# Optimization experiments

Measured on AMD Instinct MI355X. Metric: run time of the kernel, lower is better.

## Reference

```python
import jax, jax.numpy as jnp
import numpy as np

N_GRAPHS = 256
NEG_SLOPE = 0.2


def _add_self_loops(src, dst, edge_attr, n):
    # PyG fill_value='mean': self-loop edge_attr = per-node mean of incoming edge_attr
    sums = jax.ops.segment_sum(edge_attr, dst, num_segments=n)
    cnt = jax.ops.segment_sum(jnp.ones((dst.shape[0],), edge_attr.dtype), dst, num_segments=n)
    loop_attr = sums / jnp.maximum(cnt, 1.0)[:, None]
    loop = jnp.arange(n)
    src = jnp.concatenate([src, loop])
    dst = jnp.concatenate([dst, loop])
    ea = jnp.concatenate([edge_attr, loop_attr], axis=0)
    return src, dst, ea


def _segment_softmax(scores, seg, n):
    # scores: [E, H]; softmax over edges sharing the same target node
    m = jax.ops.segment_max(scores, seg, num_segments=n)
    ex = jnp.exp(scores - m[seg])
    s = jax.ops.segment_sum(ex, seg, num_segments=n)
    return ex / jnp.maximum(s[seg], 1e-16)


def gatv2_layer(x, src, dst, ea, w_l, w_r, w_e, att, b, heads, out_ch, concat):
    n = x.shape[0]
    x_l = (x @ w_l).reshape(n, heads, out_ch)  # source transform
    x_r = (x @ w_r).reshape(n, heads, out_ch)  # target transform
    e_f = (ea @ w_e).reshape(-1, heads, out_ch)
    m = x_l[src] + x_r[dst] + e_f                               # [E, H, C]
    score = jnp.einsum('ehc,hc->eh', jax.nn.leaky_relu(m, NEG_SLOPE), att)
    alpha = _segment_softmax(score, dst, n)                      # [E, H]
    out = jax.ops.segment_sum(alpha[:, :, None] * x_l[src], dst, num_segments=n)
    if concat:
        return out.reshape(n, heads * out_ch) + b
    return out.mean(axis=1) + b


def reference(x, edge_index, edge_attr, batch,
              w_l1, w_r1, w_e1, att1, b1,
              w_l2, w_r2, w_e2, att2, b2,
              w_fc, b_fc):
    n = x.shape[0]
    src, dst, ea = _add_self_loops(edge_index[0], edge_index[1], edge_attr, n)
    h = gatv2_layer(x, src, dst, ea, w_l1, w_r1, w_e1, att1, b1, heads=2, out_ch=32, concat=True)
    h = jax.nn.relu(h)
    h = gatv2_layer(h, src, dst, ea, w_l2, w_r2, w_e2, att2, b2, heads=1, out_ch=32, concat=False)
    h = jax.nn.relu(h)
    # global mean pool over graphs
    sums = jax.ops.segment_sum(h, batch, num_segments=N_GRAPHS)
    cnt = jax.ops.segment_sum(jnp.ones((n,), h.dtype), batch, num_segments=N_GRAPHS)
    pooled = sums / jnp.maximum(cnt, 1.0)[:, None]
    return pooled @ w_fc + b_fc


def setup_inputs() -> dict:
    key = jax.random.key(0)
    ks = jax.random.split(key, 20)
    N, E, IN, H, C, ED, OUT = 100000, 1600000, 128, 2, 32, 16, 32
    s = 0.05
    return {
        'x': jax.random.normal(ks[0], (N, IN), jnp.float32),
        'edge_index': jax.random.randint(ks[1], (2, E), 0, N, jnp.int32),
        'edge_attr': jax.random.normal(ks[2], (E, ED), jnp.float32),
        'batch': jnp.sort(jax.random.randint(ks[3], (N,), 0, 256, jnp.int32)),
        'w_l1': jax.random.normal(ks[4], (IN, H * C), jnp.float32) * s,
        'w_r1': jax.random.normal(ks[5], (IN, H * C), jnp.float32) * s,
        'w_e1': jax.random.normal(ks[6], (ED, H * C), jnp.float32) * s,
        'att1': jax.random.normal(ks[7], (H, C), jnp.float32) * s,
        'b1': jnp.zeros((H * C,), jnp.float32),
        'w_l2': jax.random.normal(ks[8], (H * C, C), jnp.float32) * s,
        'w_r2': jax.random.normal(ks[9], (H * C, C), jnp.float32) * s,
        'w_e2': jax.random.normal(ks[10], (ED, C), jnp.float32) * s,
        'att2': jax.random.normal(ks[11], (1, C), jnp.float32) * s,
        'b2': jnp.zeros((C,), jnp.float32),
        'w_fc': jax.random.normal(ks[12], (C, OUT), jnp.float32) * s,
        'b_fc': jnp.zeros((OUT,), jnp.float32),
    }
```

## Files before the change

### kernel.cpp

```cpp
#include <hip/hip_runtime.h>
#include <hip/hip_bf16.h>
#include <hip/hip_fp16.h>

#define NEG_SLOPE 0.2f
#define LOG2E 1.4426950408889634f

typedef _Float16 h2v __attribute__((ext_vector_type(2)));
typedef __fp16 f16x2 __attribute__((ext_vector_type(2)));
union hu { h2v h; f16x2 f; unsigned int u; };

__global__ void scan1_k(const int* __restrict__ deg, int* __restrict__ rowptr,
                        int* __restrict__ aux, int N) {
  __shared__ int sh[256];
  int t = threadIdx.x, i = blockIdx.x * 256 + t;
  int v = (i < N) ? deg[i] : 0;
  sh[t] = v; __syncthreads();
  for (int off = 1; off < 256; off <<= 1) {
    int x = (t >= off) ? sh[t - off] : 0;
    __syncthreads();
    sh[t] += x;
    __syncthreads();
  }
  if (i < N) rowptr[i] = sh[t] - v;
  if (t == 255) aux[blockIdx.x] = sh[255];
}

__global__ void scan2_k(int* __restrict__ aux, int naux) {
  __shared__ int sh[512];
  int t = threadIdx.x;
  int v = (t < naux) ? aux[t] : 0;
  sh[t] = v; __syncthreads();
  for (int off = 1; off < 512; off <<= 1) {
    int x = (t >= off) ? sh[t - off] : 0;
    __syncthreads();
    sh[t] += x;
    __syncthreads();
  }
  if (t < naux) aux[t] = sh[t] - v;
}

__global__ void scan3_k(int* __restrict__ rowptr, int* __restrict__ cursor,
                        const int* __restrict__ aux, int N, int E) {
  int i = blockIdx.x * blockDim.x + threadIdx.x;
  if (i < N) {
    int r = rowptr[i] + aux[i >> 8];
    rowptr[i] = r;
    cursor[i] = r;
  } else if (i == N) {
    rowptr[N] = E;
  }
}

__global__ void scatter_k(const int* __restrict__ srcA, const int* __restrict__ dstA,
                          const float* __restrict__ ea, int* __restrict__ cursor,
                          int* __restrict__ csr_src, uint4* __restrict__ ea_h, int E) {
  int e = blockIdx.x * blockDim.x + threadIdx.x;
  if (e >= E) return;
  int pos = atomicAdd(&cursor[dstA[e]], 1);
  csr_src[pos] = srcA[e];
  const float* p = ea + (size_t)e * 16;
  union { __half2 h2[8]; uint4 u[2]; } cv;
#pragma unroll
  for (int k = 0; k < 8; ++k) cv.h2[k] = __floats2half2_rn(p[2 * k], p[2 * k + 1]);
  uint4* d = ea_h + (size_t)pos * 2;
  d[0] = cv.u[0];
  d[1] = cv.u[1];
}

__global__ __launch_bounds__(256) void t1deg_k(
    const float* __restrict__ x, const float* __restrict__ wl, const float* __restrict__ wr,
    float* __restrict__ xl, float* __restrict__ xr, int N,
    const int* __restrict__ dstA, int* __restrict__ deg, int E, int degBlocks) {
  __shared__ unsigned int wS[64 * 128];
  __shared__ unsigned int xs[32 * 64];
  int t = threadIdx.x;
  if ((int)blockIdx.x < degBlocks) {
    int base = blockIdx.x * 1024 + t;
#pragma unroll
    for (int k = 0; k < 4; ++k) {
      int e = base + k * 256;
      if (e < E) atomicAdd(&deg[dstA[e]], 1);
    }
    return;
  }
  int tile = blockIdx.x - degBlocks;
  for (int i = t; i < 64 * 64; i += 256) {
    int kp = i >> 6, j = i & 63;
    hu pl, pr;
    pl.f = __builtin_amdgcn_cvt_pkrtz(wl[(2 * kp) * 64 + j], wl[(2 * kp + 1) * 64 + j]);
    pr.f = __builtin_amdgcn_cvt_pkrtz(wr[(2 * kp) * 64 + j], wr[(2 * kp + 1) * 64 + j]);
    wS[kp * 128 + j]      = pl.u;
    wS[kp * 128 + 64 + j] = pr.u;
  }
  {
    int base = tile << 5;
    const float4* x4 = (const float4*)x;
    for (int i = t; i < 1024; i += 256) {
      int node = base + (i >> 5);
      float4 v = {0.f, 0.f, 0.f, 0.f};
      if (node < N) v = x4[(size_t)node * 32 + (i & 31)];
      hu p0, p1;
      p0.f = __builtin_amdgcn_cvt_pkrtz(v.x, v.y);
      p1.f = __builtin_amdgcn_cvt_pkrtz(v.z, v.w);
      uint2* d = (uint2*)&xs[(i >> 5) * 64 + (i & 31) * 2];
      *d = make_uint2(p0.u, p1.u);
    }
    __syncthreads();
    int tc = t & 31;
    int tr = t >> 5;
    float4 acc0 = {0,0,0,0}, acc1 = {0,0,0,0}, acc2 = {0,0,0,0}, acc3 = {0,0,0,0};
    const unsigned int* xrow = &xs[tr * 4 * 64];
#pragma unroll 4
    for (int kp = 0; kp < 64; ++kp) {
      uint4 wu = *(const uint4*)&wS[kp * 128 + tc * 4];
      hu w0, w1, w2, w3, q0, q1, q2, q3;
      w0.u = wu.x; w1.u = wu.y; w2.u = wu.z; w3.u = wu.w;
      q0.u = xrow[kp]; q1.u = xrow[64 + kp]; q2.u = xrow[128 + kp]; q3.u = xrow[192 + kp];
      acc0.x = __builtin_amdgcn_fdot2(q0.h, w0.h, acc0.x, false);
      acc0.y = __builtin_amdgcn_fdot2(q0.h, w1.h, acc0.y, false);
      acc0.z = __builtin_amdgcn_fdot2(q0.h, w2.h, acc0.z, false);
      acc0.w = __builtin_amdgcn_fdot2(q0.h, w3.h, acc0.w, false);
      acc1.x = __builtin_amdgcn_fdot2(q1.h, w0.h, acc1.x, false);
      acc1.y = __builtin_amdgcn_fdot2(q1.h, w1.h, acc1.y, false);
      acc1.z = __builtin_amdgcn_fdot2(q1.h, w2.h, acc1.z, false);
      acc1.w = __builtin_amdgcn_fdot2(q1.h, w3.h, acc1.w, false);
      acc2.x = __builtin_amdgcn_fdot2(q2.h, w0.h, acc2.x, false);
      acc2.y = __builtin_amdgcn_fdot2(q2.h, w1.h, acc2.y, false);
      acc2.z = __builtin_amdgcn_fdot2(q2.h, w2.h, acc2.z, false);
      acc2.w = __builtin_amdgcn_fdot2(q2.h, w3.h, acc2.w, false);
      acc3.x = __builtin_amdgcn_fdot2(q3.h, w0.h, acc3.x, false);
      acc3.y = __builtin_amdgcn_fdot2(q3.h, w1.h, acc3.y, false);
      acc3.z = __builtin_amdgcn_fdot2(q3.h, w2.h, acc3.z, false);
      acc3.w = __builtin_amdgcn_fdot2(q3.h, w3.h, acc3.w, false);
    }
    float* dp = (tc < 16) ? xl : xr;
    int j4 = (tc & 15) * 4;
    int nb = base + tr * 4;
    if (nb + 0 < N) *(float4*)&dp[(size_t)(nb + 0) * 64 + j4] = acc0;
    if (nb + 1 < N) *(float4*)&dp[(size_t)(nb + 1) * 64 + j4] = acc1;
    if (nb + 2 < N) *(float4*)&dp[(size_t)(nb + 2) * 64 + j4] = acc2;
    if (nb + 3 < N) *(float4*)&dp[(size_t)(nb + 3) * 64 + j4] = acc3;
  }
}

__global__ __launch_bounds__(256) void transform2_k(
    const float* __restrict__ h, const float* __restrict__ wl, const float* __restrict__ wr,
    float* __restrict__ xl, float* __restrict__ xr, int N) {
  __shared__ unsigned int wS[32 * 64];
  __shared__ unsigned int xs[64 * 32];
  int t = threadIdx.x;
  for (int i = t; i < 32 * 32; i += 256) {
    int kp = i >> 5, j = i & 31;
    hu pl, pr;
    pl.f = __builtin_amdgcn_cvt_pkrtz(wl[(2 * kp) * 32 + j], wl[(2 * kp + 1) * 32 + j]);
    pr.f = __builtin_amdgcn_cvt_pkrtz(wr[(2 * kp) * 32 + j], wr[(2 * kp + 1) * 32 + j]);
    wS[kp * 64 + j]      = pl.u;
    wS[kp * 64 + 32 + j] = pr.u;
  }
  {
    int tile = blockIdx.x;
    int base = tile << 6;
    const float4* h4 = (const float4*)h;
    for (int i = t; i < 1024; i += 256) {
      int node = base + (i >> 4);
      float4 v = {0.f, 0.f, 0.f, 0.f};
      if (node < N) v = h4[(size_t)node * 16 + (i & 15)];
      hu p0, p1;
      p0.f = __builtin_amdgcn_cvt_pkrtz(v.x, v.y);
      p1.f = __builtin_amdgcn_cvt_pkrtz(v.z, v.w);
      uint2* d = (uint2*)&xs[(i >> 4) * 32 + (i & 15) * 2];
      *d = make_uint2(p0.u, p1.u);
    }
    __syncthreads();
    int tc = t & 15;
    int tr = t >> 4;
    float4 acc0 = {0,0,0,0}, acc1 = {0,0,0,0}, acc2 = {0,0,0,0}, acc3 = {0,0,0,0};
    const unsigned int* xrow = &xs[tr * 4 * 32];
#pragma unroll 4
    for (int kp = 0; kp < 32; ++kp) {
      uint4 wu = *(const uint4*)&wS[kp * 64 + tc * 4];
      hu w0, w1, w2, w3, q0, q1, q2, q3;
      w0.u = wu.x; w1.u = wu.y; w2.u = wu.z; w3.u = wu.w;
      q0.u = xrow[kp]; q1.u = xrow[32 + kp]; q2.u = xrow[64 + kp]; q3.u = xrow[96 + kp];
      acc0.x = __builtin_amdgcn_fdot2(q0.h, w0.h, acc0.x, false);
      acc0.y = __builtin_amdgcn_fdot2(q0.h, w1.h, acc0.y, false);
      acc0.z = __builtin_amdgcn_fdot2(q0.h, w2.h, acc0.z, false);
      acc0.w = __builtin_amdgcn_fdot2(q0.h, w3.h, acc0.w, false);
      acc1.x = __builtin_amdgcn_fdot2(q1.h, w0.h, acc1.x, false);
      acc1.y = __builtin_amdgcn_fdot2(q1.h, w1.h, acc1.y, false);
      acc1.z = __builtin_amdgcn_fdot2(q1.h, w2.h, acc1.z, false);
      acc1.w = __builtin_amdgcn_fdot2(q1.h, w3.h, acc1.w, false);
      acc2.x = __builtin_amdgcn_fdot2(q2.h, w0.h, acc2.x, false);
      acc2.y = __builtin_amdgcn_fdot2(q2.h, w1.h, acc2.y, false);
      acc2.z = __builtin_amdgcn_fdot2(q2.h, w2.h, acc2.z, false);
      acc2.w = __builtin_amdgcn_fdot2(q2.h, w3.h, acc2.w, false);
      acc3.x = __builtin_amdgcn_fdot2(q3.h, w0.h, acc3.x, false);
      acc3.y = __builtin_amdgcn_fdot2(q3.h, w1.h, acc3.y, false);
      acc3.z = __builtin_amdgcn_fdot2(q3.h, w2.h, acc3.z, false);
      acc3.w = __builtin_amdgcn_fdot2(q3.h, w3.h, acc3.w, false);
    }
    float* dp = (tc < 8) ? xl : xr;
    int j4 = (tc & 7) * 4;
    int nb = base + tr * 4;
    if (nb + 0 < N) *(float4*)&dp[(size_t)(nb + 0) * 32 + j4] = acc0;
    if (nb + 1 < N) *(float4*)&dp[(size_t)(nb + 1) * 32 + j4] = acc1;
    if (nb + 2 < N) *(float4*)&dp[(size_t)(nb + 2) * 32 + j4] = acc2;
    if (nb + 3 < N) *(float4*)&dp[(size_t)(nb + 3) * 32 + j4] = acc3;
  }
}

__global__ __launch_bounds__(256) void gat1_k(
    const int* __restrict__ rowptr, const int* __restrict__ csr_src,
    const uint4* __restrict__ ea_h, const float* __restrict__ we,
    const float* __restrict__ att, const float* __restrict__ b,
    const float* __restrict__ xl, const float* __restrict__ xr,
    float* __restrict__ h, int N) {
  int t = threadIdx.x;
  int lane = t & 63;
  h2v wh[8];
#pragma unroll
  for (int k = 0; k < 8; ++k) {
    wh[k].x = (_Float16)we[(2 * k) * 64 + lane];
    wh[k].y = (_Float16)we[(2 * k + 1) * 64 + lane];
  }
  float att_r = att[lane] * LOG2E;
  float b_r = b[lane];
  int wid = (blockIdx.x * blockDim.x + t) >> 6;
  int n0 = wid * 4;
  for (int jj = 0; jj < 4; ++jj) {
    int n = n0 + jj;
    if (n >= N) break;
    float xr_v = xr[(size_t)n * 64 + lane];
    float xl_s = xl[(size_t)n * 64 + lane];
    float num = 0.f, den = 0.f, efsum = 0.f;
    int rs = __builtin_amdgcn_readfirstlane(rowptr[n]);
    int re = __builtin_amdgcn_readfirstlane(rowptr[n + 1]);
    for (int base = rs; base < re; base += 64) {
      int cnt = min(64, re - base);
      int s_l = 0;
      if (lane < cnt) s_l = csr_src[base + lane];
      int i = 0;
      for (; i + 1 < cnt; i += 2) {
        int sa = __builtin_amdgcn_readlane(s_l, i);
        int sb = __builtin_amdgcn_readlane(s_l, i + 1);
        const float* pa = xl + (size_t)sa * 64;
        const float* pb = xl + (size_t)sb * 64;
        float xa = pa[lane];
        float xb = pb[lane];
        const uint4* epa = ea_h + (size_t)(base + i) * 2;
        union { uint4 u; h2v h[4]; } a0, a1, c0, c1;
        a0.u = epa[0]; a1.u = epa[1];
        c0.u = epa[2]; c1.u = epa[3];
        float fa0 = 0.f, fa1 = 0.f, fb0 = 0.f, fb1 = 0.f;
        fa0 = __builtin_amdgcn_fdot2(a0.h[0], wh[0], fa0, false);
        fb0 = __builtin_amdgcn_fdot2(c0.h[0], wh[0], fb0, false);
        fa1 = __builtin_amdgcn_fdot2(a0.h[1], wh[1], fa1, false);
        fb1 = __builtin_amdgcn_fdot2(c0.h[1], wh[1], fb1, false);
        fa0 = __builtin_amdgcn_fdot2(a0.h[2], wh[2], fa0, false);
        fb0 = __builtin_amdgcn_fdot2(c0.h[2], wh[2], fb0, false);
        fa1 = __builtin_amdgcn_fdot2(a0.h[3], wh[3], fa1, false);
        fb1 = __builtin_amdgcn_fdot2(c0.h[3], wh[3], fb1, false);
        fa0 = __builtin_amdgcn_fdot2(a1.h[0], wh[4], fa0, false);
        fb0 = __builtin_amdgcn_fdot2(c1.h[0], wh[4], fb0, false);
        fa1 = __builtin_amdgcn_fdot2(a1.h[1], wh[5], fa1, false);
        fb1 = __builtin_amdgcn_fdot2(c1.h[1], wh[5], fb1, false);
        fa0 = __builtin_amdgcn_fdot2(a1.h[2], wh[6], fa0, false);
        fb0 = __builtin_amdgcn_fdot2(c1.h[2], wh[6], fb0, false);
        fa1 = __builtin_amdgcn_fdot2(a1.h[3], wh[7], fa1, false);
        fb1 = __builtin_amdgcn_fdot2(c1.h[3], wh[7], fb1, false);
        float fa = fa0 + fa1, fb = fb0 + fb1;
        float ma = xa + xr_v + fa; ma = fmaxf(ma, NEG_SLOPE * ma);
        float mb = xb + xr_v + fb; mb = fmaxf(mb, NEG_SLOPE * mb);
        float ta = ma * att_r, tb = mb * att_r;
#pragma unroll
        for (int off = 1; off < 32; off <<= 1) {
          ta += __shfl_xor(ta, off);
          tb += __shfl_xor(tb, off);
        }
        float ga = __builtin_amdgcn_exp2f(ta), gb = __builtin_amdgcn_exp2f(tb);
        num += ga * xa + gb * xb;
        den += ga + gb;
        efsum += fa + fb;
      }
      if (i < cnt) {
        int sa = __builtin_amdgcn_readlane(s_l, i);
        const float* pa = xl + (size_t)sa * 64;
        float xa = pa[lane];
        const uint4* epa = ea_h + (size_t)(base + i) * 2;
        union { uint4 u; h2v h[4]; } a0, a1;
        a0.u = epa[0]; a1.u = epa[1];
        float fa0 = 0.f, fa1 = 0.f;
        fa0 = __builtin_amdgcn_fdot2(a0.h[0], wh[0], fa0, false);
        fa1 = __builtin_amdgcn_fdot2(a0.h[1], wh[1], fa1, false);
        fa0 = __builtin_amdgcn_fdot2(a0.h[2], wh[2], fa0, false);
        fa1 = __builtin_amdgcn_fdot2(a0.h[3], wh[3], fa1, false);
        fa0 = __builtin_amdgcn_fdot2(a1.h[0], wh[4], fa0, false);
        fa1 = __builtin_amdgcn_fdot2(a1.h[1], wh[5], fa1, false);
        fa0 = __builtin_amdgcn_fdot2(a1.h[2], wh[6], fa0, false);
        fa1 = __builtin_amdgcn_fdot2(a1.h[3], wh[7], fa1, false);
        float fa = fa0 + fa1;
        float ma = xa + xr_v + fa; ma = fmaxf(ma, NEG_SLOPE * ma);
        float ta = ma * att_r;
#pragma unroll
        for (int off = 1; off < 32; off <<= 1) ta += __shfl_xor(ta, off);
        float ga = __builtin_amdgcn_exp2f(ta);
        num += ga * xa;
        den += ga;
        efsum += fa;
      }
    }
    int deg = re - rs;
    float ef_self = efsum * __builtin_amdgcn_rcpf(fmaxf((float)deg, 1.f));
    float mm = xl_s + xr_v + ef_self;
    mm = fmaxf(mm, NEG_SLOPE * mm);
    float s2 = mm * att_r;
#pragma unroll
    for (int off = 1; off < 32; off <<= 1) s2 += __shfl_xor(s2, off);
    float e2 = __builtin_amdgcn_exp2f(s2);
    num += e2 * xl_s;
    den += e2;
    h[(size_t)n * 64 + lane] = fmaxf(num * __builtin_amdgcn_rcpf(fmaxf(den, 1e-16f)) + b_r, 0.f);
  }
}

__global__ __launch_bounds__(256) void gat2_k(
    const int* __restrict__ rowptr, const int* __restrict__ csr_src,
    const uint4* __restrict__ ea_h, const float* __restrict__ we,
    const float* __restrict__ att, const float* __restrict__ b,
    const float* __restrict__ xl, const float* __restrict__ xr,
    float* __restrict__ h, int N) {
  int t = threadIdx.x;
  int lane = t & 63;
  int c = lane & 31;
  int half = lane >> 5;
  int hbase = lane & 32;
  h2v wh[8];
#pragma unroll
  for (int k = 0; k < 8; ++k) {
    wh[k].x = (_Float16)we[(2 * k) * 32 + c];
    wh[k].y = (_Float16)we[(2 * k + 1) * 32 + c];
  }
  float att_r = att[c] * LOG2E;
  float b_r = b[c];
  int wid = (blockIdx.x * blockDim.x + t) >> 6;
  int p0 = wid * 4;
  for (int jj = 0; jj < 4; ++jj) {
    int p = p0 + jj;
    if (p * 2 >= N) break;
    int n = p * 2 + half;
    if (n >= N) continue;
    float xr_v = xr[(size_t)n * 32 + c];
    float xl_s = xl[(size_t)n * 32 + c];
    float num = 0.f, den = 0.f, efsum = 0.f;
    int rs = rowptr[n], re = rowptr[n + 1];
    for (int base = rs; base < re; base += 32) {
      int cnt = min(32, re - base);
      int s_l = 0;
      if (c < cnt) s_l = csr_src[base + c];
      int i = 0;
      for (; i + 1 < cnt; i += 2) {
        int sa = __shfl(s_l, hbase + i), sb = __shfl(s_l, hbase + i + 1);
        float xa = xl[(size_t)sa * 32 + c];
        float xb = xl[(size_t)sb * 32 + c];
        const uint4* epa = ea_h + (size_t)(base + i) * 2;
        union { uint4 u; h2v h[4]; } a0, a1, c0, c1;
        a0.u = epa[0]; a1.u = epa[1];
        c0.u = epa[2]; c1.u = epa[3];
        float fa0 = 0.f, fa1 = 0.f, fb0 = 0.f, fb1 = 0.f;
        fa0 = __builtin_amdgcn_fdot2(a0.h[0], wh[0], fa0, false);
        fb0 = __builtin_amdgcn_fdot2(c0.h[0], wh[0], fb0, false);
        fa1 = __builtin_amdgcn_fdot2(a0.h[1], wh[1], fa1, false);
        fb1 = __builtin_amdgcn_fdot2(c0.h[1], wh[1], fb1, false);
        fa0 = __builtin_amdgcn_fdot2(a0.h[2], wh[2], fa0, false);
        fb0 = __builtin_amdgcn_fdot2(c0.h[2], wh[2], fb0, false);
        fa1 = __builtin_amdgcn_fdot2(a0.h[3], wh[3], fa1, false);
        fb1 = __builtin_amdgcn_fdot2(c0.h[3], wh[3], fb1, false);
        fa0 = __builtin_amdgcn_fdot2(a1.h[0], wh[4], fa0, false);
        fb0 = __builtin_amdgcn_fdot2(c1.h[0], wh[4], fb0, false);
        fa1 = __builtin_amdgcn_fdot2(a1.h[1], wh[5], fa1, false);
        fb1 = __builtin_amdgcn_fdot2(c1.h[1], wh[5], fb1, false);
        fa0 = __builtin_amdgcn_fdot2(a1.h[2], wh[6], fa0, false);
        fb0 = __builtin_amdgcn_fdot2(c1.h[2], wh[6], fb0, false);
        fa1 = __builtin_amdgcn_fdot2(a1.h[3], wh[7], fa1, false);
        fb1 = __builtin_amdgcn_fdot2(c1.h[3], wh[7], fb1, false);
        float fa = fa0 + fa1, fb = fb0 + fb1;
        float ma = xa + xr_v + fa; ma = fmaxf(ma, NEG_SLOPE * ma);
        float mb = xb + xr_v + fb; mb = fmaxf(mb, NEG_SLOPE * mb);
        float ta = ma * att_r, tb = mb * att_r;
#pragma unroll
        for (int off = 1; off < 32; off <<= 1) {
          ta += __shfl_xor(ta, off);
          tb += __shfl_xor(tb, off);
        }
        float ga = __builtin_amdgcn_exp2f(ta), gb = __builtin_amdgcn_exp2f(tb);
        num += ga * xa + gb * xb;
        den += ga + gb;
        efsum += fa + fb;
      }
      if (i < cnt) {
        int sa = __shfl(s_l, hbase + i);
        float xa = xl[(size_t)sa * 32 + c];
        const uint4* epa = ea_h + (size_t)(base + i) * 2;
        union { uint4 u; h2v h[4]; } a0, a1;
        a0.u = epa[0]; a1.u = epa[1];
        float fa0 = 0.f, fa1 = 0.f;
        fa0 = __builtin_amdgcn_fdot2(a0.h[0], wh[0], fa0, false);
        fa1 = __builtin_amdgcn_fdot2(a0.h[1], wh[1], fa1, false);
        fa0 = __builtin_amdgcn_fdot2(a0.h[2], wh[2], fa0, false);
        fa1 = __builtin_amdgcn_fdot2(a0.h[3], wh[3], fa1, false);
        fa0 = __builtin_amdgcn_fdot2(a1.h[0], wh[4], fa0, false);
        fa1 = __builtin_amdgcn_fdot2(a1.h[1], wh[5], fa1, false);
        fa0 = __builtin_amdgcn_fdot2(a1.h[2], wh[6], fa0, false);
        fa1 = __builtin_amdgcn_fdot2(a1.h[3], wh[7], fa1, false);
        float fa = fa0 + fa1;
        float ma = xa + xr_v + fa; ma = fmaxf(ma, NEG_SLOPE * ma);
        float ta = ma * att_r;
#pragma unroll
        for (int off = 1; off < 32; off <<= 1) ta += __shfl_xor(ta, off);
        float ga = __builtin_amdgcn_exp2f(ta);
        num += ga * xa;
        den += ga;
        efsum += fa;
      }
    }
    int deg = re - rs;
    float ef_self = efsum * __builtin_amdgcn_rcpf(fmaxf((float)deg, 1.f));
    float mm = xl_s + xr_v + ef_self;
    mm = fmaxf(mm, NEG_SLOPE * mm);
    float s2 = mm * att_r;
#pragma unroll
    for (int off = 1; off < 32; off <<= 1) s2 += __shfl_xor(s2, off);
    float e2 = __builtin_amdgcn_exp2f(s2);
    num += e2 * xl_s;
    den += e2;
    h[(size_t)n * 32 + c] = fmaxf(num * __builtin_amdgcn_rcpf(fmaxf(den, 1e-16f)) + b_r, 0.f);
  }
}

__global__ __launch_bounds__(256) void pool_fc_k(
    const float* __restrict__ h, const int* __restrict__ batch,
    const float* __restrict__ wfc, const float* __restrict__ bfc,
    float* __restrict__ out, int N) {
  int g = blockIdx.x;
  __shared__ int srange[2];
  __shared__ float part[8][32];
  int t = threadIdx.x;
  if (t < 2) {
    int key = g + t;
    int lo = 0, hi = N;
    while (lo < hi) { int mid = (lo + hi) >> 1; if (batch[mid] < key) lo = mid + 1; else hi = mid; }
    srange[t] = lo;
  }
  __syncthreads();
  int rs = srange[0], re = srange[1];
  int c = t & 31, sub = t >> 5;
  float acc = 0.f;
  for (int n = rs + sub; n < re; n += 8) acc += h[(size_t)n * 32 + c];
  part[sub][c] = acc;
  __syncthreads();
  if (sub == 0) {
    float s = part[0][c];
#pragma unroll
    for (int i = 1; i < 8; ++i) s += part[i][c];
    part[0][c] = s / fmaxf((float)(re - rs), 1.f);
  }
  __syncthreads();
  if (sub == 0) {
    float a = 0.f;
#pragma unroll
    for (int k = 0; k < 32; ++k) a += part[0][k] * wfc[k * 32 + c];
    out[g * 32 + c] = a + bfc[c];
  }
}

extern "C" void kernel_launch(void* const* d_in, const int* in_sizes, int n_in,
                              void* d_out, int out_size, void* d_ws, size_t ws_size,
                              hipStream_t stream) {
  const float* x   = (const float*)d_in[0];
  const int*   ei  = (const int*)d_in[1];
  const float* ea  = (const float*)d_in[2];
  const int*   bat = (const int*)d_in[3];
  const float* wl1 = (const float*)d_in[4];
  const float* wr1 = (const float*)d_in[5];
  const float* we1 = (const float*)d_in[6];
  const float* at1 = (const float*)d_in[7];
  const float* b1  = (const float*)d_in[8];
  const float* wl2 = (const float*)d_in[9];
  const float* wr2 = (const float*)d_in[10];
  const float* we2 = (const float*)d_in[11];
  const float* at2 = (const float*)d_in[12];
  const float* b2  = (const float*)d_in[13];
  const float* wfc = (const float*)d_in[14];
  const float* bfc = (const float*)d_in[15];

  const int N = in_sizes[0] / 128;
  const int E = in_sizes[1] / 2;
  const int G = 256;
  const int* srcA = ei;
  const int* dstA = ei + E;

  uint4* ea_h   = (uint4*)d_ws;
  float* xl1    = (float*)(ea_h + (size_t)E * 2);
  float* xr1    = xl1 + (size_t)N * 64;
  int*   deg    = (int*)(xr1 + (size_t)N * 64);
  int*   rowptr = deg + N;
  int*   cursor = rowptr + (N + 1);
  int*   aux    = cursor + N;
  int*   csr_src= aux + 512;
  float* h1     = xr1;
  float* xl2    = xl1;
  float* xr2    = xl1 + (size_t)N * 32;
  float* h2     = xr2;

  const int naux = (N + 255) / 256;
  const int degBlocks = (E + 1023) / 1024;
  const int ntiles1 = (N + 31) / 32;

  (void)hipMemsetAsync(deg, 0, (size_t)N * sizeof(int), stream);
  t1deg_k<<<degBlocks + ntiles1, 256, 0, stream>>>(x, wl1, wr1, xl1, xr1, N,
                                                   dstA, deg, E, degBlocks);
  scan1_k<<<naux, 256, 0, stream>>>(deg, rowptr, aux, N);
  scan2_k<<<1, 512, 0, stream>>>(aux, naux);
  scan3_k<<<(N + 256) / 256, 256, 0, stream>>>(rowptr, cursor, aux, N, E);
  scatter_k<<<(E + 255) / 256, 256, 0, stream>>>(srcA, dstA, ea, cursor, csr_src, ea_h, E);

  {
    int blocks1 = (N + 15) / 16;
    gat1_k<<<blocks1, 256, 0, stream>>>(rowptr, csr_src, ea_h, we1, at1, b1,
                                        xl1, xr1, h1, N);
  }

  transform2_k<<<(N + 63) / 64, 256, 0, stream>>>(h1, wl2, wr2, xl2, xr2, N);
  {
    int P = (N + 1) / 2;
    int blocks2 = (P + 15) / 16;
    gat2_k<<<blocks2, 256, 0, stream>>>(rowptr, csr_src, ea_h, we2, at2, b2,
                                        xl2, xr2, h2, N);
  }

  pool_fc_k<<<G, 256, 0, stream>>>(h2, bat, wfc, bfc, (float*)d_out, N);
}
```

Before: 480.4 us.

## Fuse layer-1 transform with CSR scatter and unroll gat1 edge loop by four

The layer-1 node transform is moved out of the degree-count kernel and merged with the CSR scatter kernel, so the dense GEMM tiles run alongside the atomic-heavy scatter instead of alongside degree counting. Degree counting becomes its own small kernel. The gat1 edge loop is unrolled from two to four edges per iteration to expose more independent gathers. A shared fp16 dot-product helper replaces duplicated code. The scatter blocks now use the 32KB-LDS kernel's resource footprint, which may lower their occupancy, and the wider unroll raises register pressure.

```diff
diff --git a/kernel.cpp b/kernel.cpp
--- a/kernel.cpp
+++ b/kernel.cpp
@@ -8,6 +8,30 @@
 typedef _Float16 h2v __attribute__((ext_vector_type(2)));
 typedef __fp16 f16x2 __attribute__((ext_vector_type(2)));
 union hu { h2v h; f16x2 f; unsigned int u; };
+
+__device__ __forceinline__ float dot16h(uint4 u0, uint4 u1, const h2v* wh) {
+  union { uint4 u; h2v h[4]; } a0, a1;
+  a0.u = u0; a1.u = u1;
+  float f0 = 0.f, f1 = 0.f;
+  f0 = __builtin_amdgcn_fdot2(a0.h[0], wh[0], f0, false);
+  f1 = __builtin_amdgcn_fdot2(a0.h[1], wh[1], f1, false);
+  f0 = __builtin_amdgcn_fdot2(a0.h[2], wh[2], f0, false);
+  f1 = __builtin_amdgcn_fdot2(a0.h[3], wh[3], f1, false);
+  f0 = __builtin_amdgcn_fdot2(a1.h[0], wh[4], f0, false);
+  f1 = __builtin_amdgcn_fdot2(a1.h[1], wh[5], f1, false);
+  f0 = __builtin_amdgcn_fdot2(a1.h[2], wh[6], f0, false);
+  f1 = __builtin_amdgcn_fdot2(a1.h[3], wh[7], f1, false);
+  return f0 + f1;
+}
+
+__global__ void deg_count_k(const int* __restrict__ dstA, int* __restrict__ deg, int E) {
+  int base = blockIdx.x * 1024 + threadIdx.x;
+#pragma unroll
+  for (int k = 0; k < 4; ++k) {
+    int e = base + k * 256;
+    if (e < E) atomicAdd(&deg[dstA[e]], 1);
+  }
+}
 
 __global__ void scan1_k(const int* __restrict__ deg, int* __restrict__ rowptr,
                         int* __restrict__ aux, int N) {
@@ -51,39 +75,31 @@
   }
 }
 
-__global__ void scatter_k(const int* __restrict__ srcA, const int* __restrict__ dstA,
-                          const float* __restrict__ ea, int* __restrict__ cursor,
-                          int* __restrict__ csr_src, uint4* __restrict__ ea_h, int E) {
-  int e = blockIdx.x * blockDim.x + threadIdx.x;
-  if (e >= E) return;
-  int pos = atomicAdd(&cursor[dstA[e]], 1);
-  csr_src[pos] = srcA[e];
-  const float* p = ea + (size_t)e * 16;
-  union { __half2 h2[8]; uint4 u[2]; } cv;
-#pragma unroll
-  for (int k = 0; k < 8; ++k) cv.h2[k] = __floats2half2_rn(p[2 * k], p[2 * k + 1]);
-  uint4* d = ea_h + (size_t)pos * 2;
-  d[0] = cv.u[0];
-  d[1] = cv.u[1];
-}
-
-__global__ __launch_bounds__(256) void t1deg_k(
+__global__ __launch_bounds__(256) void t1scat_k(
     const float* __restrict__ x, const float* __restrict__ wl, const float* __restrict__ wr,
-    float* __restrict__ xl, float* __restrict__ xr, int N,
-    const int* __restrict__ dstA, int* __restrict__ deg, int E, int degBlocks) {
+    float* __restrict__ xl, float* __restrict__ xr, int N, int ntiles1,
+    const int* __restrict__ srcA, const int* __restrict__ dstA,
+    const float* __restrict__ ea, int* __restrict__ cursor,
+    int* __restrict__ csr_src, uint4* __restrict__ ea_h, int E) {
   __shared__ unsigned int wS[64 * 128];
   __shared__ unsigned int xs[32 * 64];
   int t = threadIdx.x;
-  if ((int)blockIdx.x < degBlocks) {
-    int base = blockIdx.x * 1024 + t;
-#pragma unroll
-    for (int k = 0; k < 4; ++k) {
-      int e = base + k * 256;
-      if (e < E) atomicAdd(&deg[dstA[e]], 1);
+  if ((int)blockIdx.x >= ntiles1) {
+    int e = (blockIdx.x - ntiles1) * 256 + t;
+    if (e < E) {
+      int pos = atomicAdd(&cursor[dstA[e]], 1);
+      csr_src[pos] = srcA[e];
+      const float* p = ea + (size_t)e * 16;
+      union { __half2 h2[8]; uint4 u[2]; } cv;
+#pragma unroll
+      for (int k = 0; k < 8; ++k) cv.h2[k] = __floats2half2_rn(p[2 * k], p[2 * k + 1]);
+      uint4* d = ea_h + (size_t)pos * 2;
+      d[0] = cv.u[0];
+      d[1] = cv.u[1];
     }
     return;
   }
-  int tile = blockIdx.x - degBlocks;
+  int tile = blockIdx.x;
   for (int i = t; i < 64 * 64; i += 256) {
     int kp = i >> 6, j = i & 63;
     hu pl, pr;
@@ -158,8 +174,7 @@
     wS[kp * 64 + 32 + j] = pr.u;
   }
   {
-    int tile = blockIdx.x;
-    int base = tile << 6;
+    int base = blockIdx.x << 6;
     const float4* h4 = (const float4*)h;
     for (int i = t; i < 1024; i += 256) {
       int node = base + (i >> 4);
@@ -240,65 +255,48 @@
       int s_l = 0;
       if (lane < cnt) s_l = csr_src[base + lane];
       int i = 0;
-      for (; i + 1 < cnt; i += 2) {
+      for (; i + 3 < cnt; i += 4) {
         int sa = __builtin_amdgcn_readlane(s_l, i);
         int sb = __builtin_amdgcn_readlane(s_l, i + 1);
-        const float* pa = xl + (size_t)sa * 64;
-        const float* pb = xl + (size_t)sb * 64;
-        float xa = pa[lane];
-        float xb = pb[lane];
-        const uint4* epa = ea_h + (size_t)(base + i) * 2;
-        union { uint4 u; h2v h[4]; } a0, a1, c0, c1;
-        a0.u = epa[0]; a1.u = epa[1];
-        c0.u = epa[2]; c1.u = epa[3];
-        float fa0 = 0.f, fa1 = 0.f, fb0 = 0.f, fb1 = 0.f;
-        fa0 = __builtin_amdgcn_fdot2(a0.h[0], wh[0], fa0, false);
-        fb0 = __builtin_amdgcn_fdot2(c0.h[0], wh[0], fb0, false);
-        fa1 = __builtin_amdgcn_fdot2(a0.h[1], wh[1], fa1, false);
-        fb1 = __builtin_amdgcn_fdot2(c0.h[1], wh[1], fb1, false);
-        fa0 = __builtin_amdgcn_fdot2(a0.h[2], wh[2], fa0, false);
-        fb0 = __builtin_amdgcn_fdot2(c0.h[2], wh[2], fb0, false);
-        fa1 = __builtin_amdgcn_fdot2(a0.h[3], wh[3], fa1, false);
-        fb1 = __builtin_amdgcn_fdot2(c0.h[3], wh[3], fb1, false);
-        fa0 = __builtin_amdgcn_fdot2(a1.h[0], wh[4], fa0, false);
-        fb0 = __builtin_amdgcn_fdot2(c1.h[0], wh[4], fb0, false);
-        fa1 = __builtin_amdgcn_fdot2(a1.h[1], wh[5], fa1, false);
-        fb1 = __builtin_amdgcn_fdot2(c1.h[1], wh[5], fb1, false);
-        fa0 = __builtin_amdgcn_fdot2(a1.h[2], wh[6], fa0, false);
-        fb0 = __builtin_amdgcn_fdot2(c1.h[2], wh[6], fb0, false);
-        fa1 = __builtin_amdgcn_fdot2(a1.h[3], wh[7], fa1, false);
-        fb1 = __builtin_amdgcn_fdot2(c1.h[3], wh[7], fb1, false);
-        float fa = fa0 + fa1, fb = fb0 + fb1;
+        int sc_ = __builtin_amdgcn_readlane(s_l, i + 2);
+        int sd = __builtin_amdgcn_readlane(s_l, i + 3);
+        float xa = (xl + (size_t)sa * 64)[lane];
+        float xb = (xl + (size_t)sb * 64)[lane];
+        float xc = (xl + (size_t)sc_ * 64)[lane];
+        float xd = (xl + (size_t)sd * 64)[lane];
+        const uint4* ep = ea_h + (size_t)(base + i) * 2;
+        uint4 u0 = ep[0], u1 = ep[1], u2 = ep[2], u3 = ep[3];
+        uint4 u4 = ep[4], u5 = ep[5], u6 = ep[6], u7 = ep[7];
+        float fa = dot16h(u0, u1, wh);
+        float fb = dot16h(u2, u3, wh);
+        float fc = dot16h(u4, u5, wh);
+        float fd = dot16h(u6, u7, wh);
         float ma = xa + xr_v + fa; ma = fmaxf(ma, NEG_SLOPE * ma);
         float mb = xb + xr_v + fb; mb = fmaxf(mb, NEG_SLOPE * mb);
-        float ta = ma * att_r, tb = mb * att_r;
+        float mc = xc + xr_v + fc; mc = fmaxf(mc, NEG_SLOPE * mc);
+        float md = xd + xr_v + fd; md = fmaxf(md, NEG_SLOPE * md);
+        float ta = ma * att_r, tb = mb * att_r, tc2 = mc * att_r, td = md * att_r;
 #pragma unroll
         for (int off = 1; off < 32; off <<= 1) {
-          ta += __shfl_xor(ta, off);
-          tb += __shfl_xor(tb, off);
+          ta  += __shfl_xor(ta, off);
+          tb  += __shfl_xor(tb, off);
+          tc2 += __shfl_xor(tc2, off);
+          td  += __shfl_xor(td, off);
         }
-        float ga = __builtin_amdgcn_exp2f(ta), gb = __builtin_amdgcn_exp2f(tb);
-        num += ga * xa + gb * xb;
-        den += ga + gb;
-        efsum += fa + fb;
+        float ga = __builtin_amdgcn_exp2f(ta);
+        float gb = __builtin_amdgcn_exp2f(tb);
+        float gc = __builtin_amdgcn_exp2f(tc2);
+        float gd = __builtin_amdgcn_exp2f(td);
+        num += ga * xa + gb * xb + gc * xc + gd * xd;
+        den += ga + gb + gc + gd;
+        efsum += fa + fb + fc + fd;
       }
-      if (i < cnt) {
+      for (; i < cnt; ++i) {
         int sa = __builtin_amdgcn_readlane(s_l, i);
-        const float* pa = xl + (size_t)sa * 64;
-        float xa = pa[lane];
-        const uint4* epa = ea_h + (size_t)(base + i) * 2;
-        union { uint4 u; h2v h[4]; } a0, a1;
-        a0.u = epa[0]; a1.u = epa[1];
-        float fa0 = 0.f, fa1 = 0.f;
-        fa0 = __builtin_amdgcn_fdot2(a0.h[0], wh[0], fa0, false);
-        fa1 = __builtin_amdgcn_fdot2(a0.h[1], wh[1], fa1, false);
-        fa0 = __builtin_amdgcn_fdot2(a0.h[2], wh[2], fa0, false);
-        fa1 = __builtin_amdgcn_fdot2(a0.h[3], wh[3], fa1, false);
-        fa0 = __builtin_amdgcn_fdot2(a1.h[0], wh[4], fa0, false);
-        fa1 = __builtin_amdgcn_fdot2(a1.h[1], wh[5], fa1, false);
-        fa0 = __builtin_amdgcn_fdot2(a1.h[2], wh[6], fa0, false);
-        fa1 = __builtin_amdgcn_fdot2(a1.h[3], wh[7], fa1, false);
-        float fa = fa0 + fa1;
+        float xa = (xl + (size_t)sa * 64)[lane];
+        const uint4* ep = ea_h + (size_t)(base + i) * 2;
+        uint4 u0 = ep[0], u1 = ep[1];
+        float fa = dot16h(u0, u1, wh);
         float ma = xa + xr_v + fa; ma = fmaxf(ma, NEG_SLOPE * ma);
         float ta = ma * att_r;
 #pragma unroll
@@ -363,27 +361,9 @@
         float xa = xl[(size_t)sa * 32 + c];
         float xb = xl[(size_t)sb * 32 + c];
         const uint4* epa = ea_h + (size_t)(base + i) * 2;
-        union { uint4 u; h2v h[4]; } a0, a1, c0, c1;
-        a0.u = epa[0]; a1.u = epa[1];
-        c0.u = epa[2]; c1.u = epa[3];
-        float fa0 = 0.f, fa1 = 0.f, fb0 = 0.f, fb1 = 0.f;
-        fa0 = __builtin_amdgcn_fdot2(a0.h[0], wh[0], fa0, false);
-        fb0 = __builtin_amdgcn_fdot2(c0.h[0], wh[0], fb0, false);
-        fa1 = __builtin_amdgcn_fdot2(a0.h[1], wh[1], fa1, false);
-        fb1 = __builtin_amdgcn_fdot2(c0.h[1], wh[1], fb1, false);
-        fa0 = __builtin_amdgcn_fdot2(a0.h[2], wh[2], fa0, false);
-        fb0 = __builtin_amdgcn_fdot2(c0.h[2], wh[2], fb0, false);
-        fa1 = __builtin_amdgcn_fdot2(a0.h[3], wh[3], fa1, false);
-        fb1 = __builtin_amdgcn_fdot2(c0.h[3], wh[3], fb1, false);
-        fa0 = __builtin_amdgcn_fdot2(a1.h[0], wh[4], fa0, false);
-        fb0 = __builtin_amdgcn_fdot2(c1.h[0], wh[4], fb0, false);
-        fa1 = __builtin_amdgcn_fdot2(a1.h[1], wh[5], fa1, false);
-        fb1 = __builtin_amdgcn_fdot2(c1.h[1], wh[5], fb1, false);
-        fa0 = __builtin_amdgcn_fdot2(a1.h[2], wh[6], fa0, false);
-        fb0 = __builtin_amdgcn_fdot2(c1.h[2], wh[6], fb0, false);
-        fa1 = __builtin_amdgcn_fdot2(a1.h[3], wh[7], fa1, false);
-        fb1 = __builtin_amdgcn_fdot2(c1.h[3], wh[7], fb1, false);
-        float fa = fa0 + fa1, fb = fb0 + fb1;
+        uint4 u0 = epa[0], u1 = epa[1], u2 = epa[2], u3 = epa[3];
+        float fa = dot16h(u0, u1, wh);
+        float fb = dot16h(u2, u3, wh);
         float ma = xa + xr_v + fa; ma = fmaxf(ma, NEG_SLOPE * ma);
         float mb = xb + xr_v + fb; mb = fmaxf(mb, NEG_SLOPE * mb);
         float ta = ma * att_r, tb = mb * att_r;
@@ -401,18 +381,8 @@
         int sa = __shfl(s_l, hbase + i);
         float xa = xl[(size_t)sa * 32 + c];
         const uint4* epa = ea_h + (size_t)(base + i) * 2;
-        union { uint4 u; h2v h[4]; } a0, a1;
-        a0.u = epa[0]; a1.u = epa[1];
-        float fa0 = 0.f, fa1 = 0.f;
-        fa0 = __builtin_amdgcn_fdot2(a0.h[0], wh[0], fa0, false);
-        fa1 = __builtin_amdgcn_fdot2(a0.h[1], wh[1], fa1, false);
-        fa0 = __builtin_amdgcn_fdot2(a0.h[2], wh[2], fa0, false);
-        fa1 = __builtin_amdgcn_fdot2(a0.h[3], wh[3], fa1, false);
-        fa0 = __builtin_amdgcn_fdot2(a1.h[0], wh[4], fa0, false);
-        fa1 = __builtin_amdgcn_fdot2(a1.h[1], wh[5], fa1, false);
-        fa0 = __builtin_amdgcn_fdot2(a1.h[2], wh[6], fa0, false);
-        fa1 = __builtin_amdgcn_fdot2(a1.h[3], wh[7], fa1, false);
-        float fa = fa0 + fa1;
+        uint4 u0 = epa[0], u1 = epa[1];
+        float fa = dot16h(u0, u1, wh);
         float ma = xa + xr_v + fa; ma = fmaxf(ma, NEG_SLOPE * ma);
         float ta = ma * att_r;
 #pragma unroll
@@ -513,16 +483,18 @@
   float* h2     = xr2;
 
   const int naux = (N + 255) / 256;
-  const int degBlocks = (E + 1023) / 1024;
   const int ntiles1 = (N + 31) / 32;
+  const int scatBlocks = (E + 255) / 256;
 
   (void)hipMemsetAsync(deg, 0, (size_t)N * sizeof(int), stream);
-  t1deg_k<<<degBlocks + ntiles1, 256, 0, stream>>>(x, wl1, wr1, xl1, xr1, N,
-                                                   dstA, deg, E, degBlocks);
+  deg_count_k<<<(E + 1023) / 1024, 256, 0, stream>>>(dstA, deg, E);
   scan1_k<<<naux, 256, 0, stream>>>(deg, rowptr, aux, N);
   scan2_k<<<1, 512, 0, stream>>>(aux, naux);
   scan3_k<<<(N + 256) / 256, 256, 0, stream>>>(rowptr, cursor, aux, N, E);
-  scatter_k<<<(E + 255) / 256, 256, 0, stream>>>(srcA, dstA, ea, cursor, csr_src, ea_h, E);
+
+  t1scat_k<<<ntiles1 + scatBlocks, 256, 0, stream>>>(x, wl1, wr1, xl1, xr1, N, ntiles1,
+                                                     srcA, dstA, ea, cursor,
+                                                     csr_src, ea_h, E);
 
   {
     int blocks1 = (N + 15) / 16;
```

Measured after the change: 460.9 us. -4.1%, faster.
